# Kernel tuning notes

Hardware: AMD Instinct MI355X
Metric: run time of the kernel (lower is better)

The kernel has to match this reference:

```python
import jax, jax.numpy as jnp
import numpy as np

B, S, IN, H, E, OUT = 64, 2048, 256, 512, 256, 32000


def setup_inputs() -> dict:
    key = jax.random.key(0)
    ks = jax.random.split(key, 20)
    g = lambda k, shp, fan_in: jax.random.normal(k, shp, jnp.float32) / jnp.sqrt(jnp.float32(fan_in))
    return {
        "x": jax.random.normal(ks[0], (B, IN), jnp.float32),
        "hidden": jax.random.normal(ks[1], (B, H), jnp.float32),
        "encoder_outputs": jax.random.normal(ks[2], (B, S, H), jnp.float32),
        # attention params
        "W1_w": g(ks[3], (H, E), H), "W1_b": jnp.zeros((E,), jnp.float32),
        "W2_w": g(ks[4], (H, E), H),
        "v_w": g(ks[5], (E, 1), E),
        # GRU gate params (input to gates is concat(x, context): IN+H)
        "Wxr_w": g(ks[6], (IN + H, H), IN + H), "Wxr_b": jnp.zeros((H,), jnp.float32),
        "Whr_w": g(ks[7], (H, H), H),
        "Wxz_w": g(ks[8], (IN + H, H), IN + H), "Wxz_b": jnp.zeros((H,), jnp.float32),
        "Whz_w": g(ks[9], (H, H), H),
        "Wxh_w": g(ks[10], (IN + H, H), IN + H), "Wxh_b": jnp.zeros((H,), jnp.float32),
        "Whh_w": g(ks[11], (H, H), H),
        # output projection
        "Who_w": g(ks[12], (H, OUT), H), "Who_b": jnp.zeros((OUT,), jnp.float32),
    }


def reference(x, hidden, encoder_outputs,
              W1_w, W1_b, W2_w, v_w,
              Wxr_w, Wxr_b, Whr_w,
              Wxz_w, Wxz_b, Whz_w,
              Wxh_w, Wxh_b, Whh_w,
              Who_w, Who_b):
    # Bahdanau attention
    # energy: [B, S, E]
    energy = jnp.tanh(jnp.einsum("bsh,he->bse", encoder_outputs, W1_w) + W1_b
                      + (hidden @ W2_w)[:, None, :])
    scores = jnp.einsum("bse,eo->bs", energy, v_w)          # [B, S]
    attn_weights = jax.nn.softmax(scores, axis=1)            # [B, S]
    context = jnp.einsum("bs,bsh->bh", attn_weights, encoder_outputs)  # [B, H]

    x_context = jnp.concatenate([x, context], axis=-1)       # [B, IN+H]
    reset_gate = jax.nn.sigmoid(x_context @ Wxr_w + Wxr_b + hidden @ Whr_w)
    update_gate = jax.nn.sigmoid(x_context @ Wxz_w + Wxz_b + hidden @ Whz_w)
    h_tilde = jnp.tanh(x_context @ Wxh_w + Wxh_b + (reset_gate * hidden) @ Whh_w)
    new_hidden = update_gate * hidden + (1.0 - update_gate) * h_tilde
    output = new_hidden @ Who_w + Who_b                      # [B, OUT]
    return (output, new_hidden, attn_weights)
```

## Files before the change

### kernel.cpp

```cpp
#include <hip/hip_runtime.h>

#define BB 64
#define SS 2048
#define INDIM 256
#define HH 512
#define EE 256
#define OUTD 32000

typedef __attribute__((ext_vector_type(8))) short short8;
typedef __attribute__((ext_vector_type(4))) float floatx4;

#define LOG2E 1.4426950408889634f

__device__ __forceinline__ unsigned short f2bf(float f) {
  unsigned u = __float_as_uint(f);
  return (unsigned short)((u + 0x7FFFu + ((u >> 16) & 1u)) >> 16);
}
__device__ __forceinline__ unsigned pk2(float a, float b) {
  return (unsigned)f2bf(a) | ((unsigned)f2bf(b) << 16);
}
__device__ __forceinline__ float bf2f(unsigned short u) {
  return __uint_as_float((unsigned)u << 16);
}
__device__ __forceinline__ float fast_tanh(float x) {
  float e = __builtin_amdgcn_exp2f(x * 2.8853900817779268f);
  return 1.0f - 2.0f * __builtin_amdgcn_rcpf(e + 1.0f);
}
__device__ __forceinline__ float fast_sigmoid(float x) {
  float e = __builtin_amdgcn_exp2f(-x * LOG2E);
  return __builtin_amdgcn_rcpf(1.0f + e);
}

typedef __attribute__((address_space(1))) const void g1void;
typedef __attribute__((address_space(3))) void l3void;
__device__ __forceinline__ void dma16(const void* g, void* l) {
  __builtin_amdgcn_global_load_lds((g1void*)g, (l3void*)l, 16, 0, 0);
}

#define WS_W1T   0
#define WS_HBP   262144
#define WS_CTX   786432
#define WS_NHBF  917504
#define WS_Z     983040
#define WS_RH    1114112
#define WS_GP    1245184
#define WS_NP    6488064
#define WS_CTXP  9109504
#define WS_SUMP  25886720
#define WS_ENCB  25894912

__global__ void k_prep(const float* __restrict__ W1, unsigned short* __restrict__ W1t) {
  int idx = blockIdx.x * 256 + threadIdx.x;
  int k = idx >> 8, e = idx & 255;
  W1t[e * HH + k] = f2bf(W1[idx]);
}

__global__ __launch_bounds__(256) void k_conv(const float* __restrict__ enc,
                                              unsigned short* __restrict__ encb) {
  int tid = threadIdx.x;
  int r_loc = tid >> 3, c0 = tid & 7;
  int row = blockIdx.x * 32 + r_loc;
  int rs = row & 7;
  const float* src = enc + (size_t)row * HH;
  unsigned short* dst = encb + (size_t)row * HH;
#pragma unroll
  for (int k = 0; k < 8; ++k) {
    int c = c0 + k * 8;
    float4 f0 = *(const float4*)(src + c * 8);
    float4 f1 = *(const float4*)(src + c * 8 + 4);
    uint4 w;
    w.x = pk2(f0.x, f0.y); w.y = pk2(f0.z, f0.w);
    w.z = pk2(f1.x, f1.y); w.w = pk2(f1.z, f1.w);
    *(uint4*)(dst + (c ^ rs) * 8) = w;
  }
}

__global__ __launch_bounds__(256) void k_hb(const float* __restrict__ hidden,
                                            const float* __restrict__ W2,
                                            const float* __restrict__ W1b,
                                            float* __restrict__ hbp) {
  int b0 = blockIdx.x * 4, seg = blockIdx.y, e = threadIdx.x;
  int h0 = seg * 64;
  float a0 = 0, a1 = 0, a2 = 0, a3 = 0;
  if (seg == 0) { a0 = a1 = a2 = a3 = W1b[e]; }
  for (int h = 0; h < 64; ++h) {
    float w = W2[(h0 + h) * EE + e];
    a0 += hidden[(b0 + 0) * HH + h0 + h] * w;
    a1 += hidden[(b0 + 1) * HH + h0 + h] * w;
    a2 += hidden[(b0 + 2) * HH + h0 + h] * w;
    a3 += hidden[(b0 + 3) * HH + h0 + h] * w;
  }
  float* o = hbp + (size_t)seg * BB * EE;
  o[(b0 + 0) * EE + e] = a0; o[(b0 + 1) * EE + e] = a1;
  o[(b0 + 2) * EE + e] = a2; o[(b0 + 3) * EE + e] = a3;
}

__global__ __launch_bounds__(256, 2) void k_scores(
    const unsigned short* __restrict__ encb, const unsigned short* __restrict__ W1t,
    const float* __restrict__ hbp, const float* __restrict__ vw,
    float* __restrict__ attn, float* __restrict__ ctxp, float* __restrict__ sump) {
  __shared__ unsigned short Afull[64 * 512];
  __shared__ float hb_s[EE], v_s[EE];
  __shared__ float red[4 * 64];
  __shared__ float wbuf[64];

  int tid = threadIdx.x;
  int m0 = blockIdx.x * 64;
  int b = blockIdx.x >> 5;
  int sloc = (blockIdx.x & 31) * 64;
  int lane = tid & 63, wn = tid >> 6;
  int l15 = lane & 15, quad = lane >> 4;

#pragma unroll
  for (int rr = 0; rr < 16; ++rr) {
    int r = wn * 16 + rr;
    dma16(encb + (size_t)(m0 + r) * HH + lane * 8, Afull + r * HH);
  }
  {
    float hbv = 0.0f;
#pragma unroll
    for (int s = 0; s < 8; ++s) hbv += hbp[s * BB * EE + b * EE + tid];
    hb_s[tid] = hbv;
    v_s[tid] = vw[tid];
  }
  __syncthreads();

  floatx4 acc[4][4];
#pragma unroll
  for (int i = 0; i < 4; ++i)
#pragma unroll
    for (int j = 0; j < 4; ++j) acc[i][j] = (floatx4)0.0f;

  const unsigned short* bbase = W1t + (size_t)(wn * 64) * HH;
#pragma unroll
  for (int kb = 0; kb < 16; ++kb) {
    short8 a[4];
#pragma unroll
    for (int i = 0; i < 4; ++i) {
      int r = i * 16 + l15;
      int pc = (kb * 4 + quad) ^ (l15 & 7);
      a[i] = *(const short8*)(Afull + r * HH + pc * 8);
    }
#pragma unroll
    for (int j = 0; j < 4; ++j) {
      short8 bfr = *(const short8*)(bbase + (size_t)(j * 16 + l15) * HH + kb * 32 + quad * 8);
#pragma unroll
      for (int i = 0; i < 4; ++i)
        acc[i][j] = __builtin_amdgcn_mfma_f32_16x16x32_bf16(a[i], bfr, acc[i][j], 0, 0, 0);
    }
  }
  __syncthreads();

#pragma unroll
  for (int i = 0; i < 4; ++i)
#pragma unroll
    for (int r = 0; r < 4; ++r) {
      float s = 0.0f;
#pragma unroll
      for (int j = 0; j < 4; ++j) {
        int e = wn * 64 + j * 16 + l15;
        s += fast_tanh(acc[i][j][r] + hb_s[e]) * v_s[e];
      }
#pragma unroll
      for (int off = 1; off < 16; off <<= 1) s += __shfl_xor(s, off, 64);
      if (l15 == 0) red[wn * 64 + i * 16 + quad * 4 + r] = s;
    }
  __syncthreads();
  if (tid < 64) {
    float sc = red[tid] + red[64 + tid] + red[128 + tid] + red[192 + tid];
    float e = __builtin_amdgcn_exp2f(sc * LOG2E);
    wbuf[tid] = e;
    attn[b * SS + sloc + tid] = e;
    float s = e;
#pragma unroll
    for (int off = 1; off < 64; off <<= 1) s += __shfl_xor(s, off, 64);
    if (tid == 0) sump[blockIdx.x] = s;
  }
  __syncthreads();

  float cacc[8];
#pragma unroll
  for (int j = 0; j < 8; ++j) cacc[j] = 0.0f;
#pragma unroll
  for (int rr = 0; rr < 16; ++rr) {
    int r = wn * 16 + rr;
    float w = wbuf[r];
    int pc = lane ^ (r & 7);
    short8 av = *(const short8*)(Afull + r * HH + pc * 8);
#pragma unroll
    for (int j = 0; j < 8; ++j) cacc[j] += w * bf2f((unsigned short)av[j]);
  }
  float4 c0, c1;
  c0.x = cacc[0]; c0.y = cacc[1]; c0.z = cacc[2]; c0.w = cacc[3];
  c1.x = cacc[4]; c1.y = cacc[5]; c1.z = cacc[6]; c1.w = cacc[7];
  float* cp = ctxp + ((size_t)blockIdx.x * 4 + wn) * HH + lane * 8;
  *(float4*)cp = c0;
  *(float4*)(cp + 4) = c1;
}

__global__ __launch_bounds__(512) void k_norm(float* __restrict__ attn,
                                              const float* __restrict__ ctxp,
                                              const float* __restrict__ sump,
                                              float* __restrict__ ctx) {
  int b = blockIdx.x, tid = threadIdx.x;
  float s = 0.0f;
#pragma unroll
  for (int t = 0; t < 32; ++t) s += sump[b * 32 + t];
  float inv = 1.0f / s;
#pragma unroll
  for (int i = 0; i < 4; ++i) attn[b * SS + tid + i * 512] *= inv;
  float c = 0.0f;
#pragma unroll 8
  for (int t = 0; t < 128; ++t) c += ctxp[(size_t)(b * 128 + t) * HH + tid];
  ctx[b * HH + tid] = c * inv;
}

__device__ __forceinline__ void part_seg(
    const float* __restrict__ Wx, const float* __restrict__ Wh,
    const float* __restrict__ x, const float* __restrict__ ctx,
    const float* __restrict__ hv, int seg, int b0, int h,
    float* __restrict__ outp) {
  const float* wseg;
  const float* a0; const float* a1; const float* a2; const float* a3;
  int vk0 = seg * 64;
  if (seg < 4) {
    wseg = Wx + (size_t)vk0 * HH;
    a0 = x + (b0 + 0) * INDIM + vk0;       a1 = x + (b0 + 1) * INDIM + vk0;
    a2 = x + (b0 + 2) * INDIM + vk0;       a3 = x + (b0 + 3) * INDIM + vk0;
  } else if (seg < 12) {
    wseg = Wx + (size_t)vk0 * HH;
    int off = vk0 - 256;
    a0 = ctx + (b0 + 0) * HH + off;        a1 = ctx + (b0 + 1) * HH + off;
    a2 = ctx + (b0 + 2) * HH + off;        a3 = ctx + (b0 + 3) * HH + off;
  } else {
    int off = vk0 - 768;
    wseg = Wh + (size_t)off * HH;
    a0 = hv + (b0 + 0) * HH + off;         a1 = hv + (b0 + 1) * HH + off;
    a2 = hv + (b0 + 2) * HH + off;         a3 = hv + (b0 + 3) * HH + off;
  }
  float s0 = 0, s1 = 0, s2 = 0, s3 = 0;
  for (int i = 0; i < 64; ++i) {
    float w = wseg[i * HH + h];
    s0 += a0[i] * w; s1 += a1[i] * w;
    s2 += a2[i] * w; s3 += a3[i] * w;
  }
  outp[(b0 + 0) * HH + h] = s0; outp[(b0 + 1) * HH + h] = s1;
  outp[(b0 + 2) * HH + h] = s2; outp[(b0 + 3) * HH + h] = s3;
}

__global__ __launch_bounds__(512) void k_gpart(
    const float* __restrict__ x, const float* __restrict__ ctx,
    const float* __restrict__ hidden,
    const float* __restrict__ Wxr, const float* __restrict__ Whr,
    const float* __restrict__ Wxz, const float* __restrict__ Whz,
    float* __restrict__ gp) {
  int b0 = blockIdx.x * 4, seg = blockIdx.y, sel = blockIdx.z, h = threadIdx.x;
  const float* Wx = sel ? Wxz : Wxr;
  const float* Wh = sel ? Whz : Whr;
  float* outp = gp + (size_t)(sel * 20 + seg) * BB * HH;
  part_seg(Wx, Wh, x, ctx, hidden, seg, b0, h, outp);
}

__global__ __launch_bounds__(512) void k_gred(
    const float* __restrict__ gp, const float* __restrict__ Wxrb,
    const float* __restrict__ Wxzb, const float* __restrict__ hidden,
    float* __restrict__ z_out, float* __restrict__ rh_out) {
  int b = blockIdx.x, h = threadIdx.x;
  float r = Wxrb[h], z = Wxzb[h];
#pragma unroll
  for (int s = 0; s < 20; ++s) {
    r += gp[((size_t)s * BB + b) * HH + h];
    z += gp[((size_t)(20 + s) * BB + b) * HH + h];
  }
  r = fast_sigmoid(r);
  z_out[b * HH + h] = fast_sigmoid(z);
  rh_out[b * HH + h] = r * hidden[b * HH + h];
}

__global__ __launch_bounds__(512) void k_npart(
    const float* __restrict__ x, const float* __restrict__ ctx,
    const float* __restrict__ rh,
    const float* __restrict__ Wxh, const float* __restrict__ Whh,
    float* __restrict__ np) {
  int b0 = blockIdx.x * 4, seg = blockIdx.y, h = threadIdx.x;
  float* outp = np + (size_t)seg * BB * HH;
  part_seg(Wxh, Whh, x, ctx, rh, seg, b0, h, outp);
}

__global__ __launch_bounds__(512) void k_nred(
    const float* __restrict__ np, const float* __restrict__ Wxhb,
    const float* __restrict__ z, const float* __restrict__ hidden,
    float* __restrict__ nh, unsigned short* __restrict__ nhbf) {
  int b = blockIdx.x, h = threadIdx.x;
  float a = Wxhb[h];
#pragma unroll
  for (int s = 0; s < 20; ++s) a += np[((size_t)s * BB + b) * HH + h];
  float ht = fast_tanh(a);
  float zz = z[b * HH + h];
  float val = zz * hidden[b * HH + h] + (1.0f - zz) * ht;
  nh[b * HH + h] = val;
  nhbf[b * HH + h] = f2bf(val);
}

__global__ __launch_bounds__(256) void k_out2(const unsigned short* __restrict__ nhbf,
                                              const float* __restrict__ Who,
                                              const float* __restrict__ Whob,
                                              float* __restrict__ out) {
  int tid = threadIdx.x;
  int lane = tid & 63, w = tid >> 6;
  int l15 = lane & 15, quad = lane >> 4;
  int n = blockIdx.x * 64 + w * 16 + l15;

  floatx4 acc[4];
#pragma unroll
  for (int i = 0; i < 4; ++i) acc[i] = (floatx4)0.0f;

#pragma unroll
  for (int kc = 0; kc < 16; ++kc) {
    int k0 = kc * 32;
    float bf[8];
    const float* bp = Who + (size_t)(k0 + quad * 8) * OUTD + n;
#pragma unroll
    for (int j = 0; j < 8; ++j) bf[j] = bp[(size_t)j * OUTD];
    union { unsigned u[4]; short8 v; } bu;
#pragma unroll
    for (int j = 0; j < 4; ++j) bu.u[j] = pk2(bf[2 * j], bf[2 * j + 1]);
#pragma unroll
    for (int i = 0; i < 4; ++i) {
      short8 af = *(const short8*)(nhbf + (i * 16 + l15) * HH + k0 + quad * 8);
      acc[i] = __builtin_amdgcn_mfma_f32_16x16x32_bf16(af, bu.v, acc[i], 0, 0, 0);
    }
  }
  float bias = Whob[n];
#pragma unroll
  for (int i = 0; i < 4; ++i)
#pragma unroll
    for (int r = 0; r < 4; ++r) {
      int m = i * 16 + quad * 4 + r;
      out[(size_t)m * OUTD + n] = acc[i][r] + bias;
    }
}

extern "C" void kernel_launch(void* const* d_in, const int* in_sizes, int n_in,
                              void* d_out, int out_size, void* d_ws, size_t ws_size,
                              hipStream_t stream) {
  const float* x    = (const float*)d_in[0];
  const float* hid  = (const float*)d_in[1];
  const float* enc  = (const float*)d_in[2];
  const float* W1w  = (const float*)d_in[3];
  const float* W1b  = (const float*)d_in[4];
  const float* W2w  = (const float*)d_in[5];
  const float* vw   = (const float*)d_in[6];
  const float* Wxr  = (const float*)d_in[7];
  const float* Wxrb = (const float*)d_in[8];
  const float* Whr  = (const float*)d_in[9];
  const float* Wxz  = (const float*)d_in[10];
  const float* Wxzb = (const float*)d_in[11];
  const float* Whz  = (const float*)d_in[12];
  const float* Wxh  = (const float*)d_in[13];
  const float* Wxhb = (const float*)d_in[14];
  const float* Whh  = (const float*)d_in[15];
  const float* Who  = (const float*)d_in[16];
  const float* Whob = (const float*)d_in[17];

  float* out  = (float*)d_out;
  float* nh   = out + (size_t)BB * OUTD;
  float* attn = nh + (size_t)BB * HH;

  char* ws = (char*)d_ws;
  unsigned short* W1t  = (unsigned short*)(ws + WS_W1T);
  float* hbp  = (float*)(ws + WS_HBP);
  float* ctx  = (float*)(ws + WS_CTX);
  unsigned short* nhbf = (unsigned short*)(ws + WS_NHBF);
  float* zg   = (float*)(ws + WS_Z);
  float* rh   = (float*)(ws + WS_RH);
  float* gp   = (float*)(ws + WS_GP);
  float* np   = (float*)(ws + WS_NP);
  float* ctxp = (float*)(ws + WS_CTXP);
  float* sump = (float*)(ws + WS_SUMP);
  unsigned short* encb = (unsigned short*)(ws + WS_ENCB);

  k_prep<<<512, 256, 0, stream>>>(W1w, W1t);
  k_conv<<<(BB * SS) / 32, 256, 0, stream>>>(enc, encb);
  k_hb<<<dim3(16, 8), 256, 0, stream>>>(hid, W2w, W1b, hbp);
  k_scores<<<(BB * SS) / 64, 256, 0, stream>>>(encb, W1t, hbp, vw, attn, ctxp, sump);
  k_norm<<<BB, 512, 0, stream>>>(attn, ctxp, sump, ctx);
  k_gpart<<<dim3(16, 20, 2), 512, 0, stream>>>(x, ctx, hid, Wxr, Whr, Wxz, Whz, gp);
  k_gred<<<BB, 512, 0, stream>>>(gp, Wxrb, Wxzb, hid, zg, rh);
  k_npart<<<dim3(16, 20), 512, 0, stream>>>(x, ctx, rh, Wxh, Whh, np);
  k_nred<<<BB, 512, 0, stream>>>(np, Wxhb, zg, hid, nh, nhbf);
  k_out2<<<500, 256, 0, stream>>>(nhbf, Who, Whob, out);
}
```

Baseline: 592.7 us.

## Merge prep kernels and fold gate reductions into GRU candidate and output kernels

Combines the W1 transpose, encoder bf16 conversion and hidden projection into one launch, removes the separate gate-reduction kernel by computing reset*hidden inside k_npart's hidden segments and the update gate inside k_nred, and splits k_norm/k_nred into half-width blocks for more parallelism. Adds unroll pragmas to the small dot loops. This cuts two kernel launches and the z/rh round-trips through global memory, at the cost of redundant reset-gate reduction across the 8 hidden segments of k_npart.

```diff
diff --git a/kernel.cpp b/kernel.cpp
--- a/kernel.cpp
+++ b/kernel.cpp
@@ -41,58 +41,56 @@
 #define WS_HBP   262144
 #define WS_CTX   786432
 #define WS_NHBF  917504
-#define WS_Z     983040
-#define WS_RH    1114112
 #define WS_GP    1245184
 #define WS_NP    6488064
 #define WS_CTXP  9109504
 #define WS_SUMP  25886720
 #define WS_ENCB  25894912
 
-__global__ void k_prep(const float* __restrict__ W1, unsigned short* __restrict__ W1t) {
-  int idx = blockIdx.x * 256 + threadIdx.x;
-  int k = idx >> 8, e = idx & 255;
-  W1t[e * HH + k] = f2bf(W1[idx]);
-}
-
-__global__ __launch_bounds__(256) void k_conv(const float* __restrict__ enc,
-                                              unsigned short* __restrict__ encb) {
-  int tid = threadIdx.x;
-  int r_loc = tid >> 3, c0 = tid & 7;
-  int row = blockIdx.x * 32 + r_loc;
-  int rs = row & 7;
-  const float* src = enc + (size_t)row * HH;
-  unsigned short* dst = encb + (size_t)row * HH;
-#pragma unroll
-  for (int k = 0; k < 8; ++k) {
-    int c = c0 + k * 8;
-    float4 f0 = *(const float4*)(src + c * 8);
-    float4 f1 = *(const float4*)(src + c * 8 + 4);
-    uint4 w;
-    w.x = pk2(f0.x, f0.y); w.y = pk2(f0.z, f0.w);
-    w.z = pk2(f1.x, f1.y); w.w = pk2(f1.z, f1.w);
-    *(uint4*)(dst + (c ^ rs) * 8) = w;
-  }
-}
-
-__global__ __launch_bounds__(256) void k_hb(const float* __restrict__ hidden,
-                                            const float* __restrict__ W2,
-                                            const float* __restrict__ W1b,
-                                            float* __restrict__ hbp) {
-  int b0 = blockIdx.x * 4, seg = blockIdx.y, e = threadIdx.x;
-  int h0 = seg * 64;
-  float a0 = 0, a1 = 0, a2 = 0, a3 = 0;
-  if (seg == 0) { a0 = a1 = a2 = a3 = W1b[e]; }
-  for (int h = 0; h < 64; ++h) {
-    float w = W2[(h0 + h) * EE + e];
-    a0 += hidden[(b0 + 0) * HH + h0 + h] * w;
-    a1 += hidden[(b0 + 1) * HH + h0 + h] * w;
-    a2 += hidden[(b0 + 2) * HH + h0 + h] * w;
-    a3 += hidden[(b0 + 3) * HH + h0 + h] * w;
-  }
-  float* o = hbp + (size_t)seg * BB * EE;
-  o[(b0 + 0) * EE + e] = a0; o[(b0 + 1) * EE + e] = a1;
-  o[(b0 + 2) * EE + e] = a2; o[(b0 + 3) * EE + e] = a3;
+__global__ __launch_bounds__(256) void k_pre(
+    const float* __restrict__ enc, unsigned short* __restrict__ encb,
+    const float* __restrict__ W1, unsigned short* __restrict__ W1t,
+    const float* __restrict__ hidden, const float* __restrict__ W2,
+    const float* __restrict__ W1b, float* __restrict__ hbp) {
+  int blk = blockIdx.x, tid = threadIdx.x;
+  if (blk < 4096) {
+    int r_loc = tid >> 3, c0 = tid & 7;
+    int row = blk * 32 + r_loc;
+    int rs = row & 7;
+    const float* src = enc + (size_t)row * HH;
+    unsigned short* dst = encb + (size_t)row * HH;
+#pragma unroll
+    for (int k = 0; k < 8; ++k) {
+      int c = c0 + k * 8;
+      float4 f0 = *(const float4*)(src + c * 8);
+      float4 f1 = *(const float4*)(src + c * 8 + 4);
+      uint4 w;
+      w.x = pk2(f0.x, f0.y); w.y = pk2(f0.z, f0.w);
+      w.z = pk2(f1.x, f1.y); w.w = pk2(f1.z, f1.w);
+      *(uint4*)(dst + (c ^ rs) * 8) = w;
+    }
+  } else if (blk < 4608) {
+    int idx = (blk - 4096) * 256 + tid;
+    int k = idx >> 8, e = idx & 255;
+    W1t[e * HH + k] = f2bf(W1[idx]);
+  } else {
+    int u = blk - 4608;
+    int b0 = (u & 15) * 4, seg = u >> 4, e = tid;
+    int h0 = seg * 64;
+    float a0 = 0, a1 = 0, a2 = 0, a3 = 0;
+    if (seg == 0) { a0 = a1 = a2 = a3 = W1b[e]; }
+#pragma unroll 16
+    for (int h = 0; h < 64; ++h) {
+      float w = W2[(h0 + h) * EE + e];
+      a0 += hidden[(b0 + 0) * HH + h0 + h] * w;
+      a1 += hidden[(b0 + 1) * HH + h0 + h] * w;
+      a2 += hidden[(b0 + 2) * HH + h0 + h] * w;
+      a3 += hidden[(b0 + 3) * HH + h0 + h] * w;
+    }
+    float* o = hbp + (size_t)seg * BB * EE;
+    o[(b0 + 0) * EE + e] = a0; o[(b0 + 1) * EE + e] = a1;
+    o[(b0 + 2) * EE + e] = a2; o[(b0 + 3) * EE + e] = a3;
+  }
 }
 
 __global__ __launch_bounds__(256, 2) void k_scores(
@@ -198,21 +196,22 @@
   *(float4*)(cp + 4) = c1;
 }
 
-__global__ __launch_bounds__(512) void k_norm(float* __restrict__ attn,
+__global__ __launch_bounds__(256) void k_norm(float* __restrict__ attn,
                                               const float* __restrict__ ctxp,
                                               const float* __restrict__ sump,
                                               float* __restrict__ ctx) {
-  int b = blockIdx.x, tid = threadIdx.x;
+  int b = blockIdx.x >> 1, half = blockIdx.x & 1, tid = threadIdx.x;
   float s = 0.0f;
 #pragma unroll
   for (int t = 0; t < 32; ++t) s += sump[b * 32 + t];
   float inv = 1.0f / s;
-#pragma unroll
-  for (int i = 0; i < 4; ++i) attn[b * SS + tid + i * 512] *= inv;
+  int h = half * 256 + tid;
   float c = 0.0f;
-#pragma unroll 8
-  for (int t = 0; t < 128; ++t) c += ctxp[(size_t)(b * 128 + t) * HH + tid];
-  ctx[b * HH + tid] = c * inv;
+#pragma unroll 16
+  for (int t = 0; t < 128; ++t) c += ctxp[(size_t)(b * 128 + t) * HH + h];
+  ctx[b * HH + h] = c * inv;
+#pragma unroll
+  for (int i = 0; i < 4; ++i) attn[b * SS + half * 1024 + i * 256 + tid] *= inv;
 }
 
 __device__ __forceinline__ void part_seg(
@@ -239,6 +238,7 @@
     a2 = hv + (b0 + 2) * HH + off;         a3 = hv + (b0 + 3) * HH + off;
   }
   float s0 = 0, s1 = 0, s2 = 0, s3 = 0;
+#pragma unroll 16
   for (int i = 0; i < 64; ++i) {
     float w = wseg[i * HH + h];
     s0 += a0[i] * w; s1 += a1[i] * w;
@@ -261,43 +261,66 @@
   part_seg(Wx, Wh, x, ctx, hidden, seg, b0, h, outp);
 }
 
-__global__ __launch_bounds__(512) void k_gred(
-    const float* __restrict__ gp, const float* __restrict__ Wxrb,
-    const float* __restrict__ Wxzb, const float* __restrict__ hidden,
-    float* __restrict__ z_out, float* __restrict__ rh_out) {
-  int b = blockIdx.x, h = threadIdx.x;
-  float r = Wxrb[h], z = Wxzb[h];
-#pragma unroll
-  for (int s = 0; s < 20; ++s) {
-    r += gp[((size_t)s * BB + b) * HH + h];
-    z += gp[((size_t)(20 + s) * BB + b) * HH + h];
-  }
-  r = fast_sigmoid(r);
-  z_out[b * HH + h] = fast_sigmoid(z);
-  rh_out[b * HH + h] = r * hidden[b * HH + h];
-}
-
 __global__ __launch_bounds__(512) void k_npart(
     const float* __restrict__ x, const float* __restrict__ ctx,
-    const float* __restrict__ rh,
+    const float* __restrict__ hidden, const float* __restrict__ gp,
+    const float* __restrict__ Wxrb,
     const float* __restrict__ Wxh, const float* __restrict__ Whh,
     float* __restrict__ np) {
+  __shared__ float rh_s[256];
   int b0 = blockIdx.x * 4, seg = blockIdx.y, h = threadIdx.x;
+  int vk0 = seg * 64;
+  const float* wseg;
+  const float* a0; const float* a1; const float* a2; const float* a3;
+  if (seg >= 12) {
+    int off = vk0 - 768;
+    if (h < 256) {
+      int bb = h >> 6, k = off + (h & 63);
+      float r = Wxrb[k];
+#pragma unroll
+      for (int s = 0; s < 20; ++s) r += gp[((size_t)s * BB + b0 + bb) * HH + k];
+      rh_s[h] = fast_sigmoid(r) * hidden[(b0 + bb) * HH + k];
+    }
+    __syncthreads();
+    wseg = Whh + (size_t)off * HH;
+    a0 = rh_s; a1 = rh_s + 64; a2 = rh_s + 128; a3 = rh_s + 192;
+  } else if (seg < 4) {
+    wseg = Wxh + (size_t)vk0 * HH;
+    a0 = x + (b0 + 0) * INDIM + vk0;       a1 = x + (b0 + 1) * INDIM + vk0;
+    a2 = x + (b0 + 2) * INDIM + vk0;       a3 = x + (b0 + 3) * INDIM + vk0;
+  } else {
+    int off = vk0 - 256;
+    wseg = Wxh + (size_t)vk0 * HH;
+    a0 = ctx + (b0 + 0) * HH + off;        a1 = ctx + (b0 + 1) * HH + off;
+    a2 = ctx + (b0 + 2) * HH + off;        a3 = ctx + (b0 + 3) * HH + off;
+  }
+  float s0 = 0, s1 = 0, s2 = 0, s3 = 0;
+#pragma unroll 16
+  for (int i = 0; i < 64; ++i) {
+    float w = wseg[i * HH + h];
+    s0 += a0[i] * w; s1 += a1[i] * w;
+    s2 += a2[i] * w; s3 += a3[i] * w;
+  }
   float* outp = np + (size_t)seg * BB * HH;
-  part_seg(Wxh, Whh, x, ctx, rh, seg, b0, h, outp);
-}
-
-__global__ __launch_bounds__(512) void k_nred(
-    const float* __restrict__ np, const float* __restrict__ Wxhb,
-    const float* __restrict__ z, const float* __restrict__ hidden,
+  outp[(b0 + 0) * HH + h] = s0; outp[(b0 + 1) * HH + h] = s1;
+  outp[(b0 + 2) * HH + h] = s2; outp[(b0 + 3) * HH + h] = s3;
+}
+
+__global__ __launch_bounds__(256) void k_nred(
+    const float* __restrict__ np, const float* __restrict__ gp,
+    const float* __restrict__ Wxzb, const float* __restrict__ Wxhb,
+    const float* __restrict__ hidden,
     float* __restrict__ nh, unsigned short* __restrict__ nhbf) {
-  int b = blockIdx.x, h = threadIdx.x;
+  int b = blockIdx.x >> 1, h = (blockIdx.x & 1) * 256 + threadIdx.x;
+  float z = Wxzb[h];
+#pragma unroll
+  for (int s = 0; s < 20; ++s) z += gp[((size_t)(20 + s) * BB + b) * HH + h];
+  z = fast_sigmoid(z);
   float a = Wxhb[h];
 #pragma unroll
   for (int s = 0; s < 20; ++s) a += np[((size_t)s * BB + b) * HH + h];
   float ht = fast_tanh(a);
-  float zz = z[b * HH + h];
-  float val = zz * hidden[b * HH + h] + (1.0f - zz) * ht;
+  float val = z * hidden[b * HH + h] + (1.0f - z) * ht;
   nh[b * HH + h] = val;
   nhbf[b * HH + h] = f2bf(val);
 }
@@ -372,22 +395,17 @@
   float* hbp  = (float*)(ws + WS_HBP);
   float* ctx  = (float*)(ws + WS_CTX);
   unsigned short* nhbf = (unsigned short*)(ws + WS_NHBF);
-  float* zg   = (float*)(ws + WS_Z);
-  float* rh   = (float*)(ws + WS_RH);
   float* gp   = (float*)(ws + WS_GP);
   float* np   = (float*)(ws + WS_NP);
   float* ctxp = (float*)(ws + WS_CTXP);
   float* sump = (float*)(ws + WS_SUMP);
   unsigned short* encb = (unsigned short*)(ws + WS_ENCB);
 
-  k_prep<<<512, 256, 0, stream>>>(W1w, W1t);
-  k_conv<<<(BB * SS) / 32, 256, 0, stream>>>(enc, encb);
-  k_hb<<<dim3(16, 8), 256, 0, stream>>>(hid, W2w, W1b, hbp);
+  k_pre<<<4736, 256, 0, stream>>>(enc, encb, W1w, W1t, hid, W2w, W1b, hbp);
   k_scores<<<(BB * SS) / 64, 256, 0, stream>>>(encb, W1t, hbp, vw, attn, ctxp, sump);
-  k_norm<<<BB, 512, 0, stream>>>(attn, ctxp, sump, ctx);
+  k_norm<<<128, 256, 0, stream>>>(attn, ctxp, sump, ctx);
   k_gpart<<<dim3(16, 20, 2), 512, 0, stream>>>(x, ctx, hid, Wxr, Whr, Wxz, Whz, gp);
-  k_gred<<<BB, 512, 0, stream>>>(gp, Wxrb, Wxzb, hid, zg, rh);
-  k_npart<<<dim3(16, 20), 512, 0, stream>>>(x, ctx, rh, Wxh, Whh, np);
-  k_nred<<<BB, 512, 0, stream>>>(np, Wxhb, zg, hid, nh, nhbf);
+  k_npart<<<dim3(16, 20), 512, 0, stream>>>(x, ctx, hid, gp, Wxrb, Wxh, Whh, np);
+  k_nred<<<128, 256, 0, stream>>>(np, gp, Wxzb, Wxhb, hid, nh, nhbf);
   k_out2<<<500, 256, 0, stream>>>(nhbf, Who, Whob, out);
 }
```

After: 585.1 us. About the same (-1.3%).
